# Kernel tuning notes

Measured on AMD Instinct MI355X. Metric: run time of the kernel, lower is better.

The kernel has to match this reference:

```python
import jax, jax.numpy as jnp
import numpy as np

DIM = 768
NUM_HEADS = 12
HEAD_DIM = DIM // NUM_HEADS
SCALE = HEAD_DIM ** -0.5
NEG = -9e15


def setup_inputs() -> dict:
    key = jax.random.key(0)
    ks = jax.random.split(key, 8)
    B, N, M, C = 4, 1024, 2048, DIM
    q = jax.random.normal(ks[0], (B, N, C), dtype=jnp.float32)
    kv = jax.random.normal(ks[1], (B, M, C), dtype=jnp.float32)
    mask = jax.random.randint(ks[2], (B, 1, N, M), 0, 2, dtype=jnp.int32)
    s = 1.0 / np.sqrt(C)
    Wq = jax.random.normal(ks[3], (C, C), dtype=jnp.float32) * s      # nn.Linear(dim, dim), no bias
    Wkv = jax.random.normal(ks[4], (2 * C, C), dtype=jnp.float32) * s  # nn.Linear(dim, 2*dim), no bias
    Wproj = jax.random.normal(ks[5], (C, C), dtype=jnp.float32) * s
    bproj = jax.random.normal(ks[6], (C,), dtype=jnp.float32) * s
    return {"q": q, "kv": kv, "Wq": Wq, "Wkv": Wkv, "Wproj": Wproj, "bproj": bproj, "mask": mask}


def reference(q, kv, Wq, Wkv, Wproj, bproj, mask):
    B, M, C = kv.shape
    _, N, _ = q.shape
    H, d = NUM_HEADS, HEAD_DIM
    # kv projection -> [B, M, 2, H, d] -> k, v: [B, H, M, d]
    kvp = (kv @ Wkv.T).reshape(B, M, 2, H, d)
    k = kvp[:, :, 0].transpose(0, 2, 1, 3)
    v = kvp[:, :, 1].transpose(0, 2, 1, 3)
    # q projection -> [B, H, N, d], pre-scaled
    qp = (q @ Wq.T).reshape(B, N, H, d).transpose(0, 2, 1, 3) * SCALE
    attn = jnp.einsum('bhnd,bhmd->bhnm', qp, k)  # [B, H, N, M]
    attn = jnp.where(mask == 0, NEG, attn)
    attn = jax.nn.softmax(attn, axis=-1)
    # attn_drop / proj_drop have rate 0.0 (eval): identity
    x = jnp.einsum('bhnm,bhmd->bhnd', attn, v)
    x = x.transpose(0, 2, 1, 3).reshape(B, N, C)
    x = x @ Wproj.T + bproj
    return x
```

## Files before the change

### kernel.cpp

```cpp
#include <hip/hip_runtime.h>
#include <hip/hip_bf16.h>


typedef short    s16x8  __attribute__((ext_vector_type(8)));
typedef short    s16x4  __attribute__((ext_vector_type(4)));
typedef float    f32x4  __attribute__((ext_vector_type(4)));
typedef _Float16 f16x8  __attribute__((ext_vector_type(8)));
typedef _Float16 f16x4  __attribute__((ext_vector_type(4)));
typedef _Float16 f16x2  __attribute__((ext_vector_type(2)));

#define NUM_H 12
#define DIM   768
#define NQ    1024
#define MK    2048
#define QK_SCALE_LOG2E 0.18033688f

__device__ __forceinline__ short f2h(float v) {
    _Float16 h = (_Float16)v;
    return __builtin_bit_cast(short, h);
}
__device__ __forceinline__ f32x4 mfma16x32(f16x8 a, f16x8 b, f32x4 c) {
    return __builtin_amdgcn_mfma_f32_16x16x32_f16(a, b, c, 0, 0, 0);
}
__device__ __forceinline__ f16x2 pk2h(float a, float b) {
    return __builtin_bit_cast(f16x2, __builtin_amdgcn_cvt_pkrtz(a, b));
}

__global__ __launch_bounds__(256) void prep_kernel(
    const float* __restrict__ q, const float* __restrict__ kv,
    const float* __restrict__ Wq, const float* __restrict__ Wkv,
    const float* __restrict__ Wp, const int* __restrict__ mask,
    short* __restrict__ q_h, short* __restrict__ kv_h,
    short* __restrict__ Wq_h, short* __restrict__ Wkv_h,
    short* __restrict__ Wp_h, unsigned char* __restrict__ mbytes)
{
    int bid = blockIdx.x;
    if (bid < 5760) {
        const float* s; short* d; long base;
        if (bid < 1536)      { s = q;   d = q_h;   base = (long)bid * 2048; }
        else if (bid < 4608) { s = kv;  d = kv_h;  base = (long)(bid - 1536) * 2048; }
        else if (bid < 4896) { s = Wq;  d = Wq_h;  base = (long)(bid - 4608) * 2048; }
        else if (bid < 5472) { s = Wkv; d = Wkv_h; base = (long)(bid - 4896) * 2048; }
        else                 { s = Wp;  d = Wp_h;  base = (long)(bid - 5472) * 2048; }
        long i = base + threadIdx.x * 8;
        float4 a = *(const float4*)(s + i);
        float4 b = *(const float4*)(s + i + 4);
        s16x8 r;
        r[0] = f2h(a.x); r[1] = f2h(a.y); r[2] = f2h(a.z); r[3] = f2h(a.w);
        r[4] = f2h(b.x); r[5] = f2h(b.y); r[6] = f2h(b.z); r[7] = f2h(b.w);
        *(s16x8*)(d + i) = r;
    } else {
        long base = (long)(bid - 5760) * 2048 + threadIdx.x * 8;
        int4 m0 = *(const int4*)(mask + base);
        int4 m1 = *(const int4*)(mask + base + 4);
        unsigned v = (unsigned)(m0.x != 0)        | ((unsigned)(m0.y != 0) << 1)
                   | ((unsigned)(m0.z != 0) << 2) | ((unsigned)(m0.w != 0) << 3)
                   | ((unsigned)(m1.x != 0) << 4) | ((unsigned)(m1.y != 0) << 5)
                   | ((unsigned)(m1.z != 0) << 6) | ((unsigned)(m1.w != 0) << 7);
        mbytes[base >> 3] = (unsigned char)v;
    }
}

__device__ __forceinline__ void gemm_core(
    short* smem,
    const short* __restrict__ A, const short* __restrict__ Bt,
    int Ncols, int mode, const float* __restrict__ bias,
    short* __restrict__ outb, short* __restrict__ outb2,
    float* __restrict__ outf, int bid)
{
    short (*As)[72] = (short(*)[72])smem;
    short (*Bs)[72] = (short(*)[72])(smem + 9216);

    int ntiles = Ncols >> 7;
    int m0 = (bid / ntiles) << 7;
    int n0 = (bid % ntiles) << 7;
    int t = threadIdx.x;
    int w = t >> 6, lane = t & 63, quad = lane >> 4, l16 = lane & 15;
    int wm = (w & 1) << 6, wn = (w >> 1) << 6;

    f32x4 zero4 = {0.f, 0.f, 0.f, 0.f};
    f32x4 acc[4][4];
    for (int i = 0; i < 4; i++)
        for (int j = 0; j < 4; j++) acc[i][j] = zero4;

    int lr = t >> 1;
    int lc = (t & 1) << 5;
    const short* Ap = A + (long)(m0 + lr) * DIM + lc;
    const short* Bp = Bt + (long)(n0 + lr) * DIM + lc;

    s16x8 a0[4], b0[4], a1[4], b1[4];
    #pragma unroll
    for (int c = 0; c < 4; c++) {
        a0[c] = *(const s16x8*)(Ap + c * 8);
        b0[c] = *(const s16x8*)(Bp + c * 8);
        a1[c] = *(const s16x8*)(Ap + 64 + c * 8);
        b1[c] = *(const s16x8*)(Bp + 64 + c * 8);
    }

    auto mfma_tile = [&]() {
        #pragma unroll
        for (int kh = 0; kh < 2; kh++) {
            f16x8 af[4], bfr[4];
            #pragma unroll
            for (int i = 0; i < 4; i++)
                af[i] = __builtin_bit_cast(f16x8,
                    *(const s16x8*)&As[wm + i * 16 + l16][kh * 32 + quad * 8]);
            #pragma unroll
            for (int j = 0; j < 4; j++)
                bfr[j] = __builtin_bit_cast(f16x8,
                    *(const s16x8*)&Bs[wn + j * 16 + l16][kh * 32 + quad * 8]);
            #pragma unroll
            for (int i = 0; i < 4; i++)
                #pragma unroll
                for (int j = 0; j < 4; j++)
                    acc[i][j] = mfma16x32(af[i], bfr[j], acc[i][j]);
        }
    };

    for (int kt = 0; kt < DIM; kt += 128) {
        __syncthreads();
        #pragma unroll
        for (int c = 0; c < 4; c++) {
            *(s16x8*)&As[lr][lc + c * 8] = a0[c];
            *(s16x8*)&Bs[lr][lc + c * 8] = b0[c];
        }
        __syncthreads();
        if (kt + 128 < DIM) {
            #pragma unroll
            for (int c = 0; c < 4; c++) {
                a0[c] = *(const s16x8*)(Ap + kt + 128 + c * 8);
                b0[c] = *(const s16x8*)(Bp + kt + 128 + c * 8);
            }
        }
        mfma_tile();
        __syncthreads();
        #pragma unroll
        for (int c = 0; c < 4; c++) {
            *(s16x8*)&As[lr][lc + c * 8] = a1[c];
            *(s16x8*)&Bs[lr][lc + c * 8] = b1[c];
        }
        __syncthreads();
        if (kt + 192 < DIM) {
            #pragma unroll
            for (int c = 0; c < 4; c++) {
                a1[c] = *(const s16x8*)(Ap + kt + 192 + c * 8);
                b1[c] = *(const s16x8*)(Bp + kt + 192 + c * 8);
            }
        }
        mfma_tile();
    }

    __syncthreads();

    if (mode == 2) {
        #pragma unroll
        for (int i = 0; i < 4; i++)
            #pragma unroll
            for (int j = 0; j < 4; j++)
                #pragma unroll
                for (int r = 0; r < 4; r++) {
                    int row = m0 + wm + i * 16 + quad * 4 + r;
                    int col = n0 + wn + j * 16 + l16;
                    outf[(long)row * DIM + col] = acc[i][j][r] + bias[col];
                }
        return;
    }

    short (*Cs)[136] = (short(*)[136])smem;
    bool vreg = (mode == 1) && (n0 >= DIM);

    if (!vreg) {
        float sc = (mode == 0) ? QK_SCALE_LOG2E : 1.0f;
        #pragma unroll
        for (int i = 0; i < 4; i++)
            #pragma unroll
            for (int j = 0; j < 4; j++)
                #pragma unroll
                for (int r = 0; r < 4; r++)
                    Cs[wm + i * 16 + quad * 4 + r][wn + j * 16 + l16] =
                        f2h(acc[i][j][r] * sc);
    } else {
        #pragma unroll
        for (int i = 0; i < 4; i++)
            #pragma unroll
            for (int j = 0; j < 4; j++) {
                int c = wn + j * 16 + l16;
                int r0 = wm + i * 16 + quad * 4;
                s16x4 pk;
                pk[0] = f2h(acc[i][j][0]); pk[1] = f2h(acc[i][j][1]);
                pk[2] = f2h(acc[i][j][2]); pk[3] = f2h(acc[i][j][3]);
                *(s16x4*)&Cs[c][r0] = pk;
            }
    }
    __syncthreads();

    if (!vreg) {
        int hb2 = n0 >> 6;
        long rowsN = (mode == 0) ? NQ : MK;
        int b = (int)(m0 / rowsN);
        int rb = (int)(m0 % rowsN);
        short* ob0 = outb + ((long)(b * NUM_H + hb2) * rowsN + rb) * 64;
        short* ob1 = outb + ((long)(b * NUM_H + hb2 + 1) * rowsN + rb) * 64;
        #pragma unroll
        for (int k2 = 0; k2 < 8; k2++) {
            int ch = k2 * 256 + t;
            int half = ch >> 10, off = ch & 1023;
            s16x8 vd = *(const s16x8*)&Cs[off >> 3][(half << 6) + ((off & 7) << 3)];
            *(s16x8*)((half ? ob1 : ob0) + off * 8) = vd;
        }
    } else {
        int hb2 = (n0 - DIM) >> 6;
        int b = m0 >> 11, rb = m0 & 2047;
        #pragma unroll
        for (int k2 = 0; k2 < 8; k2++) {
            int ch = k2 * 256 + t;
            int c = ch >> 4, woff = (ch & 15) << 3;
            s16x8 vd = *(const s16x8*)&Cs[c][woff];
            int half = c >> 6, dd = c & 63;
            *(s16x8*)(outb2 + (((long)(b * NUM_H + hb2 + half) * 64 + dd) * MK + rb) + woff) = vd;
        }
    }
}

__global__ __launch_bounds__(256) void gemm12_kernel(
    const short* __restrict__ qh, const short* __restrict__ Wqh,
    const short* __restrict__ kvh, const short* __restrict__ Wkvh,
    short* __restrict__ qp, short* __restrict__ kk, short* __restrict__ vt)
{
    __shared__ short smem[18432];
    if (blockIdx.x < 192)
        gemm_core(smem, qh, Wqh, 768, 0, nullptr, qp, nullptr, nullptr, blockIdx.x);
    else
        gemm_core(smem, kvh, Wkvh, 1536, 1, nullptr, kk, vt, nullptr, blockIdx.x - 192);
}

__global__ __launch_bounds__(256) void gemm3_kernel(
    const short* __restrict__ xb, const short* __restrict__ Wph,
    const float* __restrict__ bias, float* __restrict__ out)
{
    __shared__ short smem[18432];
    gemm_core(smem, xb, Wph, 768, 2, bias, nullptr, nullptr, out, blockIdx.x);
}

__global__ __launch_bounds__(256) void attn_kernel(
    const short* __restrict__ qp, const short* __restrict__ kk,
    const short* __restrict__ vt, const unsigned* __restrict__ mb,
    float* __restrict__ po0, float* __restrict__ po1, float* __restrict__ pl)
{
    __shared__ short qs[64][72];
    __shared__ short ks[64][64];
    __shared__ short vs[64][64];

    int bid = blockIdx.x;
    int bh = bid % 48;
    int rest = bid / 48;
    int nt = rest & 15;
    int half = rest >> 4;
    int h = bh % NUM_H, b = bh / NUM_H;
    int n0 = nt << 6;
    int mstart = half << 10;
    int t = threadIdx.x, w = t >> 6, lane = t & 63, quad = lane >> 4, l16 = lane & 15;
    (void)h;

    const short* qbase = qp + ((long)bh * NQ + n0) * 64;
    const short* kbase = kk + (long)bh * MK * 64;
    const short* vbase = vt + (long)bh * 64 * MK;
    const unsigned* mrow = mb + ((long)b * NQ + n0 + (w << 4) + l16) * 64;

    {
        int qr = t >> 2, c0q = (t & 3) << 4;
        *(s16x8*)&qs[qr][c0q]     = *(const s16x8*)(qbase + qr * 64 + c0q);
        *(s16x8*)&qs[qr][c0q + 8] = *(const s16x8*)(qbase + qr * 64 + c0q + 8);
    }
    __syncthreads();
    f16x8 bq[2];
    #pragma unroll
    for (int kh = 0; kh < 2; kh++)
        bq[kh] = __builtin_bit_cast(f16x8,
            *(const s16x8*)&qs[(w << 4) + l16][kh * 32 + quad * 8]);

    int sr = t >> 2, c0 = (t & 3) << 4;
    int pr = (sr & 32) + ((sr & 4) << 2) + ((sr & 24) >> 1) + (sr & 3);
    int swk = (pr & 7) << 3;
    int swv = (sr & 7) << 3;
    int swl = (l16 & 7) << 3;
    const short* kp = kbase + (long)(mstart + sr) * 64 + c0;
    const short* vp = vbase + (long)sr * MK + mstart + c0;

    s16x8 k0 = *(const s16x8*)(kp);
    s16x8 k1 = *(const s16x8*)(kp + 8);
    s16x8 v0 = *(const s16x8*)(vp);
    s16x8 v1 = *(const s16x8*)(vp + 8);
    uint2 mwv = *(const uint2*)(mrow + (mstart >> 5));

    f32x4 zero4 = {0.f, 0.f, 0.f, 0.f};
    f32x4 o[4], ol = zero4;
    for (int j = 0; j < 4; j++) o[j] = zero4;
    const f16x8 ones = {(_Float16)1.f, (_Float16)1.f, (_Float16)1.f, (_Float16)1.f,
                        (_Float16)1.f, (_Float16)1.f, (_Float16)1.f, (_Float16)1.f};

    for (int mt = 0; mt < 1024; mt += 64) {
        __syncthreads();
        *(s16x8*)&ks[pr][c0 ^ swk]       = k0;
        *(s16x8*)&ks[pr][(c0 + 8) ^ swk] = k1;
        *(s16x8*)&vs[sr][c0 ^ swv]       = v0;
        *(s16x8*)&vs[sr][(c0 + 8) ^ swv] = v1;
        unsigned cm0 = mwv.x, cm1 = mwv.y;
        __syncthreads();
        if (mt + 64 < 1024) {
            k0 = *(const s16x8*)(kp + (long)(mt + 64) * 64);
            k1 = *(const s16x8*)(kp + (long)(mt + 64) * 64 + 8);
            v0 = *(const s16x8*)(vp + mt + 64);
            v1 = *(const s16x8*)(vp + mt + 64 + 8);
            mwv = *(const uint2*)(mrow + ((mstart + mt + 64) >> 5));
        }

        f32x4 s[4];
        #pragma unroll
        for (int jj = 0; jj < 4; jj++) s[jj] = zero4;
        __builtin_amdgcn_s_setprio(1);
        #pragma unroll
        for (int kh = 0; kh < 2; kh++)
            #pragma unroll
            for (int jj = 0; jj < 4; jj++) {
                f16x8 ak = __builtin_bit_cast(f16x8,
                    *(const s16x8*)&ks[jj * 16 + l16][(kh * 32 + quad * 8) ^ swl]);
                s[jj] = mfma16x32(ak, bq[kh], s[jj]);
            }
        __builtin_amdgcn_s_setprio(0);

        f16x8 pa[2];
        #pragma unroll
        for (int j2 = 0; j2 < 2; j2++) {
            unsigned wsel = j2 ? cm1 : cm0;
            f16x2 pk[4];
            #pragma unroll
            for (int sub = 0; sub < 2; sub++) {
                unsigned bits = wsel >> ((quad << 3) + (sub << 2));
                const f32x4& sv = s[j2 * 2 + sub];
                float p0 = (bits & 1u)        ? __builtin_amdgcn_exp2f(sv[0]) : 0.f;
                float p1 = ((bits >> 1) & 1u) ? __builtin_amdgcn_exp2f(sv[1]) : 0.f;
                float p2 = ((bits >> 2) & 1u) ? __builtin_amdgcn_exp2f(sv[2]) : 0.f;
                float p3 = ((bits >> 3) & 1u) ? __builtin_amdgcn_exp2f(sv[3]) : 0.f;
                pk[sub * 2]     = pk2h(p0, p1);
                pk[sub * 2 + 1] = pk2h(p2, p3);
            }
            f16x4 lo = __builtin_shufflevector(pk[0], pk[1], 0, 1, 2, 3);
            f16x4 hi = __builtin_shufflevector(pk[2], pk[3], 0, 1, 2, 3);
            pa[j2] = __builtin_shufflevector(lo, hi, 0, 1, 2, 3, 4, 5, 6, 7);
        }

        __builtin_amdgcn_s_setprio(1);
        #pragma unroll
        for (int j2 = 0; j2 < 2; j2++) {
            ol = mfma16x32(pa[j2], ones, ol);
            #pragma unroll
            for (int jd = 0; jd < 4; jd++) {
                f16x8 bv = __builtin_bit_cast(f16x8,
                    *(const s16x8*)&vs[jd * 16 + l16][(j2 * 32 + quad * 8) ^ swl]);
                o[jd] = mfma16x32(pa[j2], bv, o[jd]);
            }
        }
        __builtin_amdgcn_s_setprio(0);
    }

    float* poh = (half ? po1 : po0)
               + ((long)bh * NQ + n0 + (w << 4)) * 64;
    #pragma unroll
    for (int jd = 0; jd < 4; jd++)
        #pragma unroll
        for (int rr = 0; rr < 4; rr++)
            poh[(quad * 4 + rr) * 64 + jd * 16 + l16] = o[jd][rr];
    if (l16 == 0) {
        float* plh = pl + (long)half * 48 * NQ + (long)bh * NQ + n0 + (w << 4);
        #pragma unroll
        for (int rr = 0; rr < 4; rr++)
            plh[quad * 4 + rr] = ol[rr];
    }
}

__global__ __launch_bounds__(256) void reduce_kernel(
    const float* __restrict__ po0, const float* __restrict__ po1,
    const float* __restrict__ pl, short* __restrict__ xb)
{
    int t = threadIdx.x;
    int r = t >> 3;
    int dp = (t & 7) << 3;
    long grow = (long)blockIdx.x * 32 + r;
    int bh = (int)(grow >> 10), n = (int)(grow & 1023);
    const float* p0 = po0 + grow * 64 + dp;
    const float* p1 = po1 + grow * 64 + dp;
    float l = pl[grow] + pl[(long)48 * NQ + grow];
    float inv = 1.0f / l;
    float4 a0 = *(const float4*)p0, a1 = *(const float4*)(p0 + 4);
    float4 b0 = *(const float4*)p1, b1 = *(const float4*)(p1 + 4);
    s16x8 r8;
    r8[0] = f2h((a0.x + b0.x) * inv);
    r8[1] = f2h((a0.y + b0.y) * inv);
    r8[2] = f2h((a0.z + b0.z) * inv);
    r8[3] = f2h((a0.w + b0.w) * inv);
    r8[4] = f2h((a1.x + b1.x) * inv);
    r8[5] = f2h((a1.y + b1.y) * inv);
    r8[6] = f2h((a1.z + b1.z) * inv);
    r8[7] = f2h((a1.w + b1.w) * inv);
    int b = bh / NUM_H, h = bh % NUM_H;
    *(s16x8*)(xb + ((long)(b * NQ + n) * DIM + h * 64 + dp)) = r8;
}

extern "C" void kernel_launch(void* const* d_in, const int* in_sizes, int n_in,
                              void* d_out, int out_size, void* d_ws, size_t ws_size,
                              hipStream_t stream)
{
    const float* q     = (const float*)d_in[0];
    const float* kv    = (const float*)d_in[1];
    const float* Wq    = (const float*)d_in[2];
    const float* Wkv   = (const float*)d_in[3];
    const float* Wproj = (const float*)d_in[4];
    const float* bproj = (const float*)d_in[5];
    const int*   mask  = (const int*)d_in[6];
    float* out = (float*)d_out;

    char* ws = (char*)d_ws;
    short* q_h   = (short*)ws; ws += (size_t)4096 * 768 * 2;
    short* kv_h  = (short*)ws; ws += (size_t)8192 * 768 * 2;
    short* Wq_h  = (short*)ws; ws += (size_t)768 * 768 * 2;
    short* Wkv_h = (short*)ws; ws += (size_t)1536 * 768 * 2;
    short* Wp_h  = (short*)ws; ws += (size_t)768 * 768 * 2;
    short* qp    = (short*)ws; ws += (size_t)4096 * 768 * 2;
    short* kk    = (short*)ws; ws += (size_t)8192 * 768 * 2;
    short* vt    = (short*)ws; ws += (size_t)8192 * 768 * 2;
    short* xb    = (short*)ws; ws += (size_t)4096 * 768 * 2;
    unsigned char* mbytes = (unsigned char*)ws; ws += (size_t)1 << 20;
    float* po0 = (float*)d_ws;
    float* po1 = (float*)ws; ws += (size_t)48 * 1024 * 64 * 4;
    float* pl  = (float*)ws; ws += (size_t)2 * 48 * 1024 * 4;

    prep_kernel<<<9856, 256, 0, stream>>>(q, kv, Wq, Wkv, Wproj, mask,
                                          q_h, kv_h, Wq_h, Wkv_h, Wp_h, mbytes);
    gemm12_kernel<<<960, 256, 0, stream>>>(q_h, Wq_h, kv_h, Wkv_h, qp, kk, vt);
    attn_kernel<<<1536, 256, 0, stream>>>(qp, kk, vt, (const unsigned*)mbytes,
                                          po0, po1, pl);
    reduce_kernel<<<1536, 256, 0, stream>>>(po0, po1, pl, xb);
    gemm3_kernel<<<192, 256, 0, stream>>>(xb, Wp_h, bproj, out);
}
```

Before: 220.1 us.

## Process 128 query rows per attention block to reuse K/V tiles

Each attention block now handles 128 query rows instead of 64, with each wave computing two 16-row query sub-tiles against the same K/V LDS tiles. This halves the number of blocks and the global and LDS traffic for K and V per query row, and raises MFMA work per LDS read. The cost is higher register pressure from doubled accumulators and fewer blocks (768) for occupancy and latency hiding.

```diff
diff --git a/kernel.cpp b/kernel.cpp
--- a/kernel.cpp
+++ b/kernel.cpp
@@ -247,37 +247,41 @@
     const short* __restrict__ vt, const unsigned* __restrict__ mb,
     float* __restrict__ po0, float* __restrict__ po1, float* __restrict__ pl)
 {
-    __shared__ short qs[64][72];
+    __shared__ short qs[128][72];
     __shared__ short ks[64][64];
     __shared__ short vs[64][64];
 
     int bid = blockIdx.x;
     int bh = bid % 48;
     int rest = bid / 48;
-    int nt = rest & 15;
-    int half = rest >> 4;
-    int h = bh % NUM_H, b = bh / NUM_H;
-    int n0 = nt << 6;
+    int nt = rest & 7;
+    int half = rest >> 3;
+    int b = bh / NUM_H;
+    int n0 = nt << 7;
     int mstart = half << 10;
     int t = threadIdx.x, w = t >> 6, lane = t & 63, quad = lane >> 4, l16 = lane & 15;
-    (void)h;
 
     const short* qbase = qp + ((long)bh * NQ + n0) * 64;
     const short* kbase = kk + (long)bh * MK * 64;
     const short* vbase = vt + (long)bh * 64 * MK;
-    const unsigned* mrow = mb + ((long)b * NQ + n0 + (w << 4) + l16) * 64;
+    const unsigned* mrow0 = mb + ((long)b * NQ + n0 + (w << 5) + l16) * 64;
+    const unsigned* mrow1 = mrow0 + 16 * 64;
 
     {
-        int qr = t >> 2, c0q = (t & 3) << 4;
-        *(s16x8*)&qs[qr][c0q]     = *(const s16x8*)(qbase + qr * 64 + c0q);
-        *(s16x8*)&qs[qr][c0q + 8] = *(const s16x8*)(qbase + qr * 64 + c0q + 8);
+        int qr = t >> 1, c0q = (t & 1) << 5;
+        #pragma unroll
+        for (int i = 0; i < 4; i++)
+            *(s16x8*)&qs[qr][c0q + i * 8] =
+                *(const s16x8*)(qbase + qr * 64 + c0q + i * 8);
     }
     __syncthreads();
-    f16x8 bq[2];
+    f16x8 bq[2][2];
     #pragma unroll
-    for (int kh = 0; kh < 2; kh++)
-        bq[kh] = __builtin_bit_cast(f16x8,
-            *(const s16x8*)&qs[(w << 4) + l16][kh * 32 + quad * 8]);
+    for (int qa = 0; qa < 2; qa++)
+        #pragma unroll
+        for (int kh = 0; kh < 2; kh++)
+            bq[qa][kh] = __builtin_bit_cast(f16x8,
+                *(const s16x8*)&qs[(w << 5) + (qa << 4) + l16][kh * 32 + quad * 8]);
 
     int sr = t >> 2, c0 = (t & 3) << 4;
     int pr = (sr & 32) + ((sr & 4) << 2) + ((sr & 24) >> 1) + (sr & 3);
@@ -291,11 +295,16 @@
     s16x8 k1 = *(const s16x8*)(kp + 8);
     s16x8 v0 = *(const s16x8*)(vp);
     s16x8 v1 = *(const s16x8*)(vp + 8);
-    uint2 mwv = *(const uint2*)(mrow + (mstart >> 5));
+    uint2 mwa = *(const uint2*)(mrow0 + (mstart >> 5));
+    uint2 mwb = *(const uint2*)(mrow1 + (mstart >> 5));
 
     f32x4 zero4 = {0.f, 0.f, 0.f, 0.f};
-    f32x4 o[4], ol = zero4;
-    for (int j = 0; j < 4; j++) o[j] = zero4;
+    f32x4 o[2][4], ol[2];
+    #pragma unroll
+    for (int qa = 0; qa < 2; qa++) {
+        ol[qa] = zero4;
+        for (int j = 0; j < 4; j++) o[qa][j] = zero4;
+    }
     const f16x8 ones = {(_Float16)1.f, (_Float16)1.f, (_Float16)1.f, (_Float16)1.f,
                         (_Float16)1.f, (_Float16)1.f, (_Float16)1.f, (_Float16)1.f};
 
@@ -305,19 +314,22 @@
         *(s16x8*)&ks[pr][(c0 + 8) ^ swk] = k1;
         *(s16x8*)&vs[sr][c0 ^ swv]       = v0;
         *(s16x8*)&vs[sr][(c0 + 8) ^ swv] = v1;
-        unsigned cm0 = mwv.x, cm1 = mwv.y;
+        uint2 cma = mwa, cmb = mwb;
         __syncthreads();
         if (mt + 64 < 1024) {
             k0 = *(const s16x8*)(kp + (long)(mt + 64) * 64);
             k1 = *(const s16x8*)(kp + (long)(mt + 64) * 64 + 8);
             v0 = *(const s16x8*)(vp + mt + 64);
             v1 = *(const s16x8*)(vp + mt + 64 + 8);
-            mwv = *(const uint2*)(mrow + ((mstart + mt + 64) >> 5));
-        }
-
-        f32x4 s[4];
-        #pragma unroll
-        for (int jj = 0; jj < 4; jj++) s[jj] = zero4;
+            mwa = *(const uint2*)(mrow0 + ((mstart + mt + 64) >> 5));
+            mwb = *(const uint2*)(mrow1 + ((mstart + mt + 64) >> 5));
+        }
+
+        f32x4 s[2][4];
+        #pragma unroll
+        for (int qa = 0; qa < 2; qa++)
+            #pragma unroll
+            for (int jj = 0; jj < 4; jj++) s[qa][jj] = zero4;
         __builtin_amdgcn_s_setprio(1);
         #pragma unroll
         for (int kh = 0; kh < 2; kh++)
@@ -325,57 +337,71 @@
             for (int jj = 0; jj < 4; jj++) {
                 f16x8 ak = __builtin_bit_cast(f16x8,
                     *(const s16x8*)&ks[jj * 16 + l16][(kh * 32 + quad * 8) ^ swl]);
-                s[jj] = mfma16x32(ak, bq[kh], s[jj]);
+                s[0][jj] = mfma16x32(ak, bq[0][kh], s[0][jj]);
+                s[1][jj] = mfma16x32(ak, bq[1][kh], s[1][jj]);
             }
         __builtin_amdgcn_s_setprio(0);
 
-        f16x8 pa[2];
+        f16x8 pa[2][2];
+        #pragma unroll
+        for (int qa = 0; qa < 2; qa++) {
+            uint2 cm = qa ? cmb : cma;
+            #pragma unroll
+            for (int j2 = 0; j2 < 2; j2++) {
+                unsigned wsel = j2 ? cm.y : cm.x;
+                f16x2 pk[4];
+                #pragma unroll
+                for (int sub = 0; sub < 2; sub++) {
+                    unsigned bits = wsel >> ((quad << 3) + (sub << 2));
+                    const f32x4& sv = s[qa][j2 * 2 + sub];
+                    float p0 = (bits & 1u)        ? __builtin_amdgcn_exp2f(sv[0]) : 0.f;
+                    float p1 = ((bits >> 1) & 1u) ? __builtin_amdgcn_exp2f(sv[1]) : 0.f;
+                    float p2 = ((bits >> 2) & 1u) ? __builtin_amdgcn_exp2f(sv[2]) : 0.f;
+                    float p3 = ((bits >> 3) & 1u) ? __builtin_amdgcn_exp2f(sv[3]) : 0.f;
+                    pk[sub * 2]     = pk2h(p0, p1);
+                    pk[sub * 2 + 1] = pk2h(p2, p3);
+                }
+                f16x4 lo = __builtin_shufflevector(pk[0], pk[1], 0, 1, 2, 3);
+                f16x4 hi = __builtin_shufflevector(pk[2], pk[3], 0, 1, 2, 3);
+                pa[qa][j2] = __builtin_shufflevector(lo, hi, 0, 1, 2, 3, 4, 5, 6, 7);
+            }
+        }
+
+        __builtin_amdgcn_s_setprio(1);
         #pragma unroll
         for (int j2 = 0; j2 < 2; j2++) {
-            unsigned wsel = j2 ? cm1 : cm0;
-            f16x2 pk[4];
-            #pragma unroll
-            for (int sub = 0; sub < 2; sub++) {
-                unsigned bits = wsel >> ((quad << 3) + (sub << 2));
-                const f32x4& sv = s[j2 * 2 + sub];
-                float p0 = (bits & 1u)        ? __builtin_amdgcn_exp2f(sv[0]) : 0.f;
-                float p1 = ((bits >> 1) & 1u) ? __builtin_amdgcn_exp2f(sv[1]) : 0.f;
-                float p2 = ((bits >> 2) & 1u) ? __builtin_amdgcn_exp2f(sv[2]) : 0.f;
-                float p3 = ((bits >> 3) & 1u) ? __builtin_amdgcn_exp2f(sv[3]) : 0.f;
-                pk[sub * 2]     = pk2h(p0, p1);
-                pk[sub * 2 + 1] = pk2h(p2, p3);
-            }
-            f16x4 lo = __builtin_shufflevector(pk[0], pk[1], 0, 1, 2, 3);
-            f16x4 hi = __builtin_shufflevector(pk[2], pk[3], 0, 1, 2, 3);
-            pa[j2] = __builtin_shufflevector(lo, hi, 0, 1, 2, 3, 4, 5, 6, 7);
-        }
-
-        __builtin_amdgcn_s_setprio(1);
-        #pragma unroll
-        for (int j2 = 0; j2 < 2; j2++) {
-            ol = mfma16x32(pa[j2], ones, ol);
+            ol[0] = mfma16x32(pa[0][j2], ones, ol[0]);
+            ol[1] = mfma16x32(pa[1][j2], ones, ol[1]);
             #pragma unroll
             for (int jd = 0; jd < 4; jd++) {
                 f16x8 bv = __builtin_bit_cast(f16x8,
                     *(const s16x8*)&vs[jd * 16 + l16][(j2 * 32 + quad * 8) ^ swl]);
-                o[jd] = mfma16x32(pa[j2], bv, o[jd]);
+                o[0][jd] = mfma16x32(pa[0][j2], bv, o[0][jd]);
+                o[1][jd] = mfma16x32(pa[1][j2], bv, o[1][jd]);
             }
         }
         __builtin_amdgcn_s_setprio(0);
     }
 
-    float* poh = (half ? po1 : po0)
-               + ((long)bh * NQ + n0 + (w << 4)) * 64;
     #pragma unroll
-    for (int jd = 0; jd < 4; jd++)
-        #pragma unroll
-        for (int rr = 0; rr < 4; rr++)
-            poh[(quad * 4 + rr) * 64 + jd * 16 + l16] = o[jd][rr];
+    for (int qa = 0; qa < 2; qa++) {
+        float* poh = (half ? po1 : po0)
+                   + ((long)bh * NQ + n0 + (w << 5) + (qa << 4)) * 64;
+        #pragma unroll
+        for (int jd = 0; jd < 4; jd++)
+            #pragma unroll
+            for (int rr = 0; rr < 4; rr++)
+                poh[(quad * 4 + rr) * 64 + jd * 16 + l16] = o[qa][jd][rr];
+    }
     if (l16 == 0) {
-        float* plh = pl + (long)half * 48 * NQ + (long)bh * NQ + n0 + (w << 4);
-        #pragma unroll
-        for (int rr = 0; rr < 4; rr++)
-            plh[quad * 4 + rr] = ol[rr];
+        #pragma unroll
+        for (int qa = 0; qa < 2; qa++) {
+            float* plh = pl + (long)half * 48 * NQ + (long)bh * NQ
+                       + n0 + (w << 5) + (qa << 4);
+            #pragma unroll
+            for (int rr = 0; rr < 4; rr++)
+                plh[quad * 4 + rr] = ol[qa][rr];
+        }
     }
 }
 
@@ -438,8 +464,8 @@
     prep_kernel<<<9856, 256, 0, stream>>>(q, kv, Wq, Wkv, Wproj, mask,
                                           q_h, kv_h, Wq_h, Wkv_h, Wp_h, mbytes);
     gemm12_kernel<<<960, 256, 0, stream>>>(q_h, Wq_h, kv_h, Wkv_h, qp, kk, vt);
-    attn_kernel<<<1536, 256, 0, stream>>>(qp, kk, vt, (const unsigned*)mbytes,
-                                          po0, po1, pl);
+    attn_kernel<<<768, 256, 0, stream>>>(qp, kk, vt, (const unsigned*)mbytes,
+                                         po0, po1, pl);
     reduce_kernel<<<1536, 256, 0, stream>>>(po0, po1, pl, xb);
     gemm3_kernel<<<192, 256, 0, stream>>>(xb, Wp_h, bproj, out);
 }
```

Measured after the change: 214.1 us. 1.03x faster.
